# Optimization experiments

Hardware: AMD Instinct MI355X
Metric: run time of the kernel (lower is better)

The kernel has to match this reference:

```python
import jax, jax.numpy as jnp
import numpy as np

NUM_HEADS = 8
NEG_INF = -2**32 + 1  # matches the TF code's masking constant


def setup_inputs() -> dict:
    key = jax.random.key(0)
    ks = jax.random.split(key, 12)
    B, L, D_IN, D_MODEL = 2, 2048, 256, 256
    s = 1.0 / np.sqrt(D_IN)
    return {
        "queries": jax.random.normal(ks[0], (B, L, D_IN), jnp.float32),
        "keys": jax.random.normal(ks[1], (B, L, D_IN), jnp.float32),
        "values": jax.random.normal(ks[2], (B, L, D_IN), jnp.float32),
        "key_mask": jax.random.randint(ks[3], (B, L, 1), 0, 2, jnp.int32),
        "Wq": jax.random.normal(ks[4], (D_IN, D_MODEL), jnp.float32) * s,
        "bq": jnp.zeros((D_MODEL,), jnp.float32),
        "Wk": jax.random.normal(ks[5], (D_IN, D_MODEL), jnp.float32) * s,
        "bk": jnp.zeros((D_MODEL,), jnp.float32),
        "Wv": jax.random.normal(ks[6], (D_IN, D_MODEL), jnp.float32) * s,
        "bv": jnp.zeros((D_MODEL,), jnp.float32),
        "Wo": jax.random.normal(ks[7], (D_MODEL, D_IN), jnp.float32) * s,
        "bo": jnp.zeros((D_IN,), jnp.float32),
    }


def reference(queries, keys, values, key_mask, Wq, bq, Wk, bk, Wv, bv, Wo, bo):
    B, Lq, _ = queries.shape
    Lk = keys.shape[1]
    h = NUM_HEADS
    d_model = Wq.shape[1]
    depth = d_model // h

    Q = queries @ Wq + bq  # [B, Lq, d_model]
    K = keys @ Wk + bk     # [B, Lk, d_model]
    V = values @ Wv + bv   # [B, Lk, d_model]

    # split heads: contiguous chunks of size depth along feature dim
    Qh = Q.reshape(B, Lq, h, depth)
    Kh = K.reshape(B, Lk, h, depth)
    Vh = V.reshape(B, Lk, h, depth)

    scores = jnp.einsum("bqhd,bkhd->bhqk", Qh, Kh) / jnp.sqrt(
        jnp.asarray(depth, jnp.float32)
    )  # [B, h, Lq, Lk]

    # key_mask: [B, Lk, 1] -> broadcast over heads and query positions
    mask = (key_mask[:, None, :, 0] != 0)[:, :, None, :]  # [B, 1, 1, Lk]
    scores = jnp.where(mask, scores, jnp.asarray(NEG_INF, scores.dtype))

    attn = jax.nn.softmax(scores, axis=-1)  # dropout is identity at inference
    out = jnp.einsum("bhqk,bkhd->bqhd", attn, Vh).reshape(B, Lq, d_model)
    return out @ Wo + bo  # [B, Lq, input_dim]
```

## Files before the change

### kernel.cpp

```cpp
#include <hip/hip_runtime.h>

#define Bn 2
#define Ln 2048
#define DIN 256
#define Hn 8
#define DEPTH 32
#define SCALE 0.17677669529663687f
#define NEGC (-4294967296.0f)
#define NG  (Ln / 16)
#define WLS 264

typedef _Float16 f16;
typedef _Float16 h8 __attribute__((ext_vector_type(8)));
typedef _Float16 h4 __attribute__((ext_vector_type(4)));
typedef float f4 __attribute__((ext_vector_type(4)));


__global__ __launch_bounds__(256) void proj_gemm(
    const float* __restrict__ Xq, const float* __restrict__ Xk, const float* __restrict__ Xv,
    const float* __restrict__ Wq, const float* __restrict__ Wk, const float* __restrict__ Wv,
    const float* __restrict__ bq, const float* __restrict__ bk, const float* __restrict__ bv,
    f16* __restrict__ Qz, f16* __restrict__ Kz, f16* __restrict__ Vz)
{
    __shared__ f16 Wl[64 * WLS];
    const int p = blockIdx.z;
    const float* X = p == 0 ? Xq : p == 1 ? Xk : Xv;
    const float* W = p == 0 ? Wq : p == 1 ? Wk : Wv;
    const float* bias = p == 0 ? bq : p == 1 ? bk : bv;

    const int t = threadIdx.x, w = t >> 6, lane = t & 63;
    const int l15 = lane & 15, quad = lane >> 4;
    const int n0 = blockIdx.y * 64;

    {
        const int nl = t & 63, kb = t >> 6;
        for (int kk = 0; kk < 64; ++kk) {
            const int k = kk * 4 + kb;
            Wl[nl * WLS + k] = (f16)W[(size_t)k * DIN + n0 + nl];
        }
    }
    __syncthreads();

    const int m0w = blockIdx.x * 128 + w * 32;
    const float* A0 = X + (size_t)(m0w + l15) * DIN;
    const float* A1 = X + (size_t)(m0w + 16 + l15) * DIN;

    f4 acc[2][4];
    #pragma unroll
    for (int mi = 0; mi < 2; ++mi)
        #pragma unroll
        for (int tt = 0; tt < 4; ++tt) acc[mi][tt] = (f4){0.f, 0.f, 0.f, 0.f};

    for (int k0 = 0; k0 < DIN; k0 += 32) {
        float4 xa0 = *(const float4*)(A0 + k0 + quad * 8);
        float4 xb0 = *(const float4*)(A0 + k0 + quad * 8 + 4);
        float4 xa1 = *(const float4*)(A1 + k0 + quad * 8);
        float4 xb1 = *(const float4*)(A1 + k0 + quad * 8 + 4);
        h8 af0 = { (f16)xa0.x, (f16)xa0.y, (f16)xa0.z, (f16)xa0.w,
                   (f16)xb0.x, (f16)xb0.y, (f16)xb0.z, (f16)xb0.w };
        h8 af1 = { (f16)xa1.x, (f16)xa1.y, (f16)xa1.z, (f16)xa1.w,
                   (f16)xb1.x, (f16)xb1.y, (f16)xb1.z, (f16)xb1.w };
        #pragma unroll
        for (int tt = 0; tt < 4; ++tt) {
            h8 bf = *(const h8*)(Wl + (tt * 16 + l15) * WLS + k0 + quad * 8);
            acc[0][tt] = __builtin_amdgcn_mfma_f32_16x16x32_f16(af0, bf, acc[0][tt], 0, 0, 0);
            acc[1][tt] = __builtin_amdgcn_mfma_f32_16x16x32_f16(af1, bf, acc[1][tt], 0, 0, 0);
        }
    }
    #pragma unroll
    for (int mi = 0; mi < 2; ++mi)
        #pragma unroll
        for (int tt = 0; tt < 4; ++tt) {
            const int c = n0 + tt * 16 + l15;
            const float bb = bias[c];
            const int h = c >> 5, dd = c & 31;
            #pragma unroll
            for (int r = 0; r < 4; ++r) {
                const int row = m0w + mi * 16 + quad * 4 + r;
                const int b = row >> 11, l = row & (Ln - 1);
                const float v = acc[mi][tt][r] + bb;
                const size_t hbg = (size_t)(b * Hn + h) * NG + (l >> 4);
                if (p == 0)
                    Qz[(hbg * 64 + (dd >> 3) * 16 + (l & 15)) * 8 + (dd & 7)] =
                        (f16)(v * SCALE);
                else if (p == 1)
                    Kz[(hbg * 64 + (dd >> 3) * 16 + (l & 15)) * 8 + (dd & 7)] = (f16)v;
                else
                    Vz[((hbg * 2 + (dd >> 4)) * 64 + ((l & 15) >> 2) * 16 + (dd & 15)) * 4
                       + (l & 3)] = (f16)v;
            }
        }
}

__global__ __launch_bounds__(256) void flash_mfma(
    const f16* __restrict__ Qz, const f16* __restrict__ Kz,
    const f16* __restrict__ Vz, const int* __restrict__ mask,
    f16* __restrict__ Oz)
{
    __shared__ float Os[4][32][34];
    __shared__ float lS[4][32];
    const int t = threadIdx.x, w = t >> 6, lane = t & 63;
    const int l15 = lane & 15, quad = lane >> 4;
    const int qc = blockIdx.x, hb = blockIdx.y;
    const int q0 = qc * 32;
    const int b = hb >> 3, h = hb & 7;
    const f16* Qh = Qz + (size_t)hb * NG * 512;
    const f16* Kh = Kz + (size_t)hb * NG * 512;
    const f16* Vh = Vz + (size_t)hb * NG * 512;
    const int* mrow = mask + b * Ln;
    const int k_base = w * (Ln / 4);

    h8 qf[2];
    #pragma unroll
    for (int qg = 0; qg < 2; ++qg)
        qf[qg] = *(const h8*)(Qh + ((size_t)(qc * 2 + qg) * 64 + lane) * 8);

    f4 o[2][2];
    #pragma unroll
    for (int i = 0; i < 2; ++i)
        #pragma unroll
        for (int j = 0; j < 2; ++j) o[i][j] = (f4){0.f, 0.f, 0.f, 0.f};
    float l_run[2] = {0.f, 0.f};

    for (int kt = 0; kt < Ln / 4 / 64; ++kt) {
        const int k0 = k_base + kt * 64;
        #pragma unroll
        for (int tt = 0; tt < 4; ++tt) {
            const int g = (k0 >> 4) + tt;
            h8 kf = *(const h8*)(Kh + ((size_t)g * 64 + lane) * 8);
            const int4 mk = *(const int4*)(mrow + g * 16 + quad * 4);
            f4 bias4 = { mk.x ? 0.f : NEGC, mk.y ? 0.f : NEGC,
                         mk.z ? 0.f : NEGC, mk.w ? 0.f : NEGC };
            h4 va0 = *(const h4*)(Vh + ((size_t)(g * 2)     * 64 + lane) * 4);
            h4 va1 = *(const h4*)(Vh + ((size_t)(g * 2 + 1) * 64 + lane) * 4);
            f4 s[2];
            #pragma unroll
            for (int qg = 0; qg < 2; ++qg)
                s[qg] = __builtin_amdgcn_mfma_f32_16x16x32_f16(kf, qf[qg], bias4, 0, 0, 0);
            #pragma unroll
            for (int qg = 0; qg < 2; ++qg) {
                h4 pf;
                #pragma unroll
                for (int r = 0; r < 4; ++r) {
                    const float pv = __expf(s[qg][r]);
                    l_run[qg] += pv;
                    pf[r] = (f16)pv;
                }
                o[0][qg] = __builtin_amdgcn_mfma_f32_16x16x16f16(va0, pf, o[0][qg], 0, 0, 0);
                o[1][qg] = __builtin_amdgcn_mfma_f32_16x16x16f16(va1, pf, o[1][qg], 0, 0, 0);
            }
        }
    }
    #pragma unroll
    for (int qg = 0; qg < 2; ++qg) {
        l_run[qg] += __shfl_xor(l_run[qg], 16, 64);
        l_run[qg] += __shfl_xor(l_run[qg], 32, 64);
        if (quad == 0) lS[w][qg * 16 + l15] = l_run[qg];
        #pragma unroll
        for (int dg = 0; dg < 2; ++dg)
            #pragma unroll
            for (int r = 0; r < 4; ++r)
                Os[w][dg * 16 + quad * 4 + r][qg * 16 + l15] = o[dg][qg][r];
    }
    __syncthreads();

    if (t < 128) {
        const int cq = t & 31, dv = t >> 5;
        const float ls = lS[0][cq] + lS[1][cq] + lS[2][cq] + lS[3][cq];
        const float inv = 1.0f / ls;
        h8 pack;
        #pragma unroll
        for (int i = 0; i < 8; ++i) {
            const int dd = dv * 8 + i;
            const float ov = Os[0][dd][cq] + Os[1][dd][cq] +
                             Os[2][dd][cq] + Os[3][dd][cq];
            pack[i] = (f16)(ov * inv);
        }
        const int gm = b * NG + ((q0 + cq) >> 4);
        *(h8*)(Oz + (((size_t)gm * 8 + h) * 64 + dv * 16 + (cq & 15)) * 8) = pack;
    }
}

__global__ __launch_bounds__(256) void out_gemm(
    const f16* __restrict__ Oz, const float* __restrict__ Wo,
    const float* __restrict__ bo, float* __restrict__ out)
{
    const int t = threadIdx.x, w = t >> 6, lane = t & 63;
    const int l15 = lane & 15, quad = lane >> 4;
    const int g = blockIdx.x;

    h8 af[8];
    #pragma unroll
    for (int h = 0; h < 8; ++h)
        af[h] = *(const h8*)(Oz + (((size_t)g * 8 + h) * 64 + lane) * 8);

    const float* Wop = Wo + w * 64 + l15;
    f4 acc[4] = {{0.f,0.f,0.f,0.f},{0.f,0.f,0.f,0.f},
                 {0.f,0.f,0.f,0.f},{0.f,0.f,0.f,0.f}};
    #pragma unroll
    for (int h = 0; h < 8; ++h) {
        h8 bf[4];
        #pragma unroll
        for (int tt = 0; tt < 4; ++tt)
            #pragma unroll
            for (int j = 0; j < 8; ++j)
                bf[tt][j] = (f16)Wop[(size_t)(h * 32 + quad * 8 + j) * DIN + tt * 16];
        #pragma unroll
        for (int tt = 0; tt < 4; ++tt)
            acc[tt] = __builtin_amdgcn_mfma_f32_16x16x32_f16(af[h], bf[tt], acc[tt], 0, 0, 0);
    }
    #pragma unroll
    for (int tt = 0; tt < 4; ++tt) {
        const int c = w * 64 + tt * 16 + l15;
        const float bb = bo[c];
        #pragma unroll
        for (int r = 0; r < 4; ++r)
            out[(size_t)(g * 16 + quad * 4 + r) * DIN + c] = acc[tt][r] + bb;
    }
}

__global__ __launch_bounds__(256) void fb_projKV(
    const float* __restrict__ Xk, const float* __restrict__ Xv,
    const float* __restrict__ Wk, const float* __restrict__ Wv,
    const float* __restrict__ bk, const float* __restrict__ bv,
    f16* S, int b)
{
    __shared__ f16 Wl[64 * WLS];
    const int p = blockIdx.z;
    const float* X = (p ? Xv : Xk) + (size_t)b * Ln * DIN;
    const float* W = p ? Wv : Wk;
    const float* bias = p ? bv : bk;

    const int t = threadIdx.x, w = t >> 6, lane = t & 63;
    const int l15 = lane & 15, quad = lane >> 4;
    const int n0 = blockIdx.y * 64;

    {
        const int nl = t & 63, kb = t >> 6;
        for (int kk = 0; kk < 64; ++kk) {
            const int k = kk * 4 + kb;
            Wl[nl * WLS + k] = (f16)W[(size_t)k * DIN + n0 + nl];
        }
    }
    __syncthreads();

    const int m0w = blockIdx.x * 128 + w * 32;
    const float* A0 = X + (size_t)(m0w + l15) * DIN;
    const float* A1 = X + (size_t)(m0w + 16 + l15) * DIN;

    f4 acc[2][4];
    #pragma unroll
    for (int mi = 0; mi < 2; ++mi)
        #pragma unroll
        for (int tt = 0; tt < 4; ++tt) acc[mi][tt] = (f4){0.f, 0.f, 0.f, 0.f};

    for (int k0 = 0; k0 < DIN; k0 += 32) {
        float4 xa0 = *(const float4*)(A0 + k0 + quad * 8);
        float4 xb0 = *(const float4*)(A0 + k0 + quad * 8 + 4);
        float4 xa1 = *(const float4*)(A1 + k0 + quad * 8);
        float4 xb1 = *(const float4*)(A1 + k0 + quad * 8 + 4);
        h8 af0 = { (f16)xa0.x, (f16)xa0.y, (f16)xa0.z, (f16)xa0.w,
                   (f16)xb0.x, (f16)xb0.y, (f16)xb0.z, (f16)xb0.w };
        h8 af1 = { (f16)xa1.x, (f16)xa1.y, (f16)xa1.z, (f16)xa1.w,
                   (f16)xb1.x, (f16)xb1.y, (f16)xb1.z, (f16)xb1.w };
        #pragma unroll
        for (int tt = 0; tt < 4; ++tt) {
            h8 bf = *(const h8*)(Wl + (tt * 16 + l15) * WLS + k0 + quad * 8);
            acc[0][tt] = __builtin_amdgcn_mfma_f32_16x16x32_f16(af0, bf, acc[0][tt], 0, 0, 0);
            acc[1][tt] = __builtin_amdgcn_mfma_f32_16x16x32_f16(af1, bf, acc[1][tt], 0, 0, 0);
        }
    }
    #pragma unroll
    for (int mi = 0; mi < 2; ++mi)
        #pragma unroll
        for (int tt = 0; tt < 4; ++tt) {
            const int c = n0 + tt * 16 + l15;
            const float bb = bias[c];
            const int h = c >> 5, dd = c & 31;
            #pragma unroll
            for (int r = 0; r < 4; ++r) {
                const int l = m0w + mi * 16 + quad * 4 + r;
                const float v = acc[mi][tt][r] + bb;
                const unsigned hg = (unsigned)h * 128 + (l >> 4);
                unsigned j;
                if (!p)
                    j = (hg * 64 + (unsigned)(dd >> 3) * 16 + (l & 15)) * 8 + (dd & 7);
                else
                    j = 524288u + ((hg * 2 + (dd >> 4)) * 64
                        + (unsigned)((l & 15) >> 2) * 16 + (dd & 15)) * 4 + (l & 3);
                S[(((size_t)(j >> 12)) << 13) + 4096u + (j & 4095u)] = (f16)v;
            }
        }
}

__global__ __launch_bounds__(512) void fb_flashQ(
    const float* __restrict__ Xq, const float* __restrict__ Wq,
    const float* __restrict__ bq, const int* __restrict__ mask,
    float* outbuf, int b)
{
    __shared__ union {
        struct { f16 Wlq[32 * WLS]; f16 Qs[2048]; } a;
        struct { float Os[8][32][68]; float lS[8][64]; } c;
    } sm;
    f16* S = (f16*)outbuf;
    const int t = threadIdx.x, w = t >> 6, lane = t & 63;
    const int l15 = lane & 15, quad = lane >> 4;
    const int h = blockIdx.x, q0 = blockIdx.y * 64;

    {
        const int nl = t & 31, kb = t >> 5;
        for (int kk = 0; kk < 16; ++kk) {
            const int k = kk * 16 + kb;
            sm.a.Wlq[nl * WLS + k] = (f16)Wq[(size_t)k * DIN + h * 32 + nl];
        }
    }
    __syncthreads();

    if (w < 4) {
        const float* A0 = Xq + (size_t)(b * Ln + q0 + w * 16 + l15) * DIN;
        f4 a2[2] = { {0.f,0.f,0.f,0.f}, {0.f,0.f,0.f,0.f} };
        #pragma unroll
        for (int kk = 0; kk < 8; ++kk) {
            const int k0 = kk * 32;
            float4 xa = *(const float4*)(A0 + k0 + quad * 8);
            float4 xb = *(const float4*)(A0 + k0 + quad * 8 + 4);
            h8 af = { (f16)xa.x, (f16)xa.y, (f16)xa.z, (f16)xa.w,
                      (f16)xb.x, (f16)xb.y, (f16)xb.z, (f16)xb.w };
            #pragma unroll
            for (int tt = 0; tt < 2; ++tt) {
                h8 bf = *(const h8*)(sm.a.Wlq + (tt * 16 + l15) * WLS + k0 + quad * 8);
                a2[tt] = __builtin_amdgcn_mfma_f32_16x16x32_f16(af, bf, a2[tt], 0, 0, 0);
            }
        }
        #pragma unroll
        for (int tt = 0; tt < 2; ++tt) {
            const int c = tt * 16 + l15;
            const float bb = bq[h * 32 + c];
            #pragma unroll
            for (int r = 0; r < 4; ++r) {
                const int lc = quad * 4 + r;
                sm.a.Qs[((size_t)w * 64 + (c >> 3) * 16 + lc) * 8 + (c & 7)] =
                    (f16)((a2[tt][r] + bb) * SCALE);
            }
        }
    }
    __syncthreads();
    h8 qf[4];
    #pragma unroll
    for (int qg = 0; qg < 4; ++qg)
        qf[qg] = *(const h8*)(sm.a.Qs + ((size_t)qg * 64 + lane) * 8);
    __syncthreads();

    const int* mrow = mask + b * Ln;
    f4 o[2][4];
    #pragma unroll
    for (int i = 0; i < 2; ++i)
        #pragma unroll
        for (int j = 0; j < 4; ++j) o[i][j] = (f4){0.f, 0.f, 0.f, 0.f};
    float l_run[4] = {0.f, 0.f, 0.f, 0.f};
    const int k_base = w * (Ln / 8);

    for (int kt = 0; kt < Ln / 8 / 64; ++kt) {
        const int k0 = k_base + kt * 64;
        #pragma unroll
        for (int tt = 0; tt < 4; ++tt) {
            const int g = (k0 >> 4) + tt;
            const size_t kaddr = ((size_t)(h * 16 + (g >> 3)) << 13) + 4096u
                               + (size_t)((g & 7) * 512 + lane * 8);
            h8 kf = *(const h8*)(S + kaddr);
            const int4 mk = *(const int4*)(mrow + g * 16 + quad * 4);
            f4 bias4 = { mk.x ? 0.f : NEGC, mk.y ? 0.f : NEGC,
                         mk.z ? 0.f : NEGC, mk.w ? 0.f : NEGC };
            const size_t vaddr = ((size_t)(128 + h * 16 + (g >> 3)) << 13) + 4096u
                               + (size_t)((g & 7) * 512 + lane * 4);
            h4 va0 = *(const h4*)(S + vaddr);
            h4 va1 = *(const h4*)(S + vaddr + 256);
            f4 s_[4];
            #pragma unroll
            for (int qg = 0; qg < 4; ++qg)
                s_[qg] = __builtin_amdgcn_mfma_f32_16x16x32_f16(kf, qf[qg], bias4, 0, 0, 0);
            #pragma unroll
            for (int qg = 0; qg < 4; ++qg) {
                h4 pf;
                #pragma unroll
                for (int r = 0; r < 4; ++r) {
                    const float pv = __expf(s_[qg][r]);
                    l_run[qg] += pv;
                    pf[r] = (f16)pv;
                }
                o[0][qg] = __builtin_amdgcn_mfma_f32_16x16x16f16(va0, pf, o[0][qg], 0, 0, 0);
                o[1][qg] = __builtin_amdgcn_mfma_f32_16x16x16f16(va1, pf, o[1][qg], 0, 0, 0);
            }
        }
    }
    #pragma unroll
    for (int qg = 0; qg < 4; ++qg) {
        l_run[qg] += __shfl_xor(l_run[qg], 16, 64);
        l_run[qg] += __shfl_xor(l_run[qg], 32, 64);
        if (quad == 0) sm.c.lS[w][qg * 16 + l15] = l_run[qg];
        #pragma unroll
        for (int dg = 0; dg < 2; ++dg)
            #pragma unroll
            for (int r = 0; r < 4; ++r)
                sm.c.Os[w][dg * 16 + quad * 4 + r][qg * 16 + l15] = o[dg][qg][r];
    }
    __syncthreads();

    if (t < 256) {
        const int cq = t & 63, dv = t >> 6;
        float ls = 0.f;
        #pragma unroll
        for (int i = 0; i < 8; ++i) ls += sm.c.lS[i][cq];
        const float inv = 1.0f / ls;
        h8 pack;
        #pragma unroll
        for (int i = 0; i < 8; ++i) {
            const int dd = dv * 8 + i;
            float ov = 0.f;
            #pragma unroll
            for (int s = 0; s < 8; ++s) ov += sm.c.Os[s][dd][cq];
            pack[i] = (f16)(ov * inv);
        }
        const int gm = b * 128 + ((q0 + cq) >> 4);
        *(h8*)(S + (size_t)gm * 8192
               + (size_t)(h * 64 + dv * 16 + (cq & 15)) * 8) = pack;
    }
}

__global__ __launch_bounds__(256) void fb_outproj(
    const float* __restrict__ Wo, const float* __restrict__ bo, float* outbuf)
{
    f16* S = (f16*)outbuf;
    const int t = threadIdx.x, w = t >> 6, lane = t & 63;
    const int l15 = lane & 15, quad = lane >> 4;
    const int g = blockIdx.x;

    h8 af[8];
    #pragma unroll
    for (int h = 0; h < 8; ++h)
        af[h] = *(const h8*)(S + (size_t)g * 8192 + (size_t)(h * 64 + lane) * 8);
    __syncthreads();

    const float* Wop = Wo + w * 64 + l15;
    f4 acc[4] = {{0.f,0.f,0.f,0.f},{0.f,0.f,0.f,0.f},
                 {0.f,0.f,0.f,0.f},{0.f,0.f,0.f,0.f}};
    #pragma unroll
    for (int h = 0; h < 8; ++h) {
        h8 bf[4];
        #pragma unroll
        for (int tt = 0; tt < 4; ++tt)
            #pragma unroll
            for (int j = 0; j < 8; ++j)
                bf[tt][j] = (f16)Wop[(size_t)(h * 32 + quad * 8 + j) * DIN + tt * 16];
        #pragma unroll
        for (int tt = 0; tt < 4; ++tt)
            acc[tt] = __builtin_amdgcn_mfma_f32_16x16x32_f16(af[h], bf[tt], acc[tt], 0, 0, 0);
    }
    #pragma unroll
    for (int tt = 0; tt < 4; ++tt) {
        const int c = w * 64 + tt * 16 + l15;
        const float bb = bo[c];
        #pragma unroll
        for (int r = 0; r < 4; ++r)
            outbuf[(size_t)(g * 16 + quad * 4 + r) * DIN + c] = acc[tt][r] + bb;
    }
}

extern "C" void kernel_launch(void* const* d_in, const int* in_sizes, int n_in,
                              void* d_out, int out_size, void* d_ws, size_t ws_size,
                              hipStream_t stream) {
    (void)in_sizes; (void)n_in; (void)out_size;
    const float* Xq = (const float*)d_in[0];
    const float* Xk = (const float*)d_in[1];
    const float* Xv = (const float*)d_in[2];
    const int*  mask = (const int*)d_in[3];
    const float* Wq = (const float*)d_in[4];
    const float* bq = (const float*)d_in[5];
    const float* Wk = (const float*)d_in[6];
    const float* bk = (const float*)d_in[7];
    const float* Wv = (const float*)d_in[8];
    const float* bv = (const float*)d_in[9];
    const float* Wo = (const float*)d_in[10];
    const float* bo = (const float*)d_in[11];
    float* out = (float*)d_out;

    const size_t HB_E = (size_t)Bn * Hn * Ln * DEPTH;
    const size_t need = 4 * HB_E * sizeof(f16);

    if (ws_size >= need) {
        f16* Qz = (f16*)d_ws;
        f16* Kz = Qz + HB_E;
        f16* Vz = Kz + HB_E;
        f16* Oz = Vz + HB_E;
        proj_gemm<<<dim3(Bn * Ln / 128, DIN / 64, 3), 256, 0, stream>>>(
            Xq, Xk, Xv, Wq, Wk, Wv, bq, bk, bv, Qz, Kz, Vz);
        flash_mfma<<<dim3(Ln / 32, Bn * Hn), 256, 0, stream>>>(Qz, Kz, Vz, mask, Oz);
        out_gemm<<<Bn * Ln / 16, 256, 0, stream>>>(Oz, Wo, bo, out);
    } else {
        f16* S = (f16*)out;
        fb_projKV<<<dim3(16, 4, 2), 256, 0, stream>>>(Xk, Xv, Wk, Wv, bk, bv, S, 0);
        fb_flashQ<<<dim3(8, 32), 512, 0, stream>>>(Xq, Wq, bq, mask, out, 0);
        fb_projKV<<<dim3(16, 4, 2), 256, 0, stream>>>(Xk, Xv, Wk, Wv, bk, bv, S, 1);
        fb_flashQ<<<dim3(8, 32), 512, 0, stream>>>(Xq, Wq, bq, mask, out, 1);
        fb_outproj<<<256, 256, 0, stream>>>(Wo, bo, out);
    }
}
```

Before: 122.4 us.

## Split work finer across all three kernels and swizzle flash block order

The projection GEMM drops its shared-memory staging of W and reads W straight from global/cache per wave, halving rows per block so twice as many blocks launch. The flash kernel moves to 8 waves per block, each covering an eighth of the keys, with a 1D grid swizzled so consecutive blocks land on different XCDs. The output GEMM splits each row group's columns across two blocks. The aim is more parallelism and occupancy on a small problem, at the cost of more redundant W loads and a larger cross-wave reduction in shared memory.

```diff
diff --git a/kernel.cpp b/kernel.cpp
--- a/kernel.cpp
+++ b/kernel.cpp
@@ -22,7 +22,6 @@
     const float* __restrict__ bq, const float* __restrict__ bk, const float* __restrict__ bv,
     f16* __restrict__ Qz, f16* __restrict__ Kz, f16* __restrict__ Vz)
 {
-    __shared__ f16 Wl[64 * WLS];
     const int p = blockIdx.z;
     const float* X = p == 0 ? Xq : p == 1 ? Xk : Xv;
     const float* W = p == 0 ? Wq : p == 1 ? Wk : Wv;
@@ -31,84 +30,72 @@
     const int t = threadIdx.x, w = t >> 6, lane = t & 63;
     const int l15 = lane & 15, quad = lane >> 4;
     const int n0 = blockIdx.y * 64;
-
-    {
-        const int nl = t & 63, kb = t >> 6;
-        for (int kk = 0; kk < 64; ++kk) {
-            const int k = kk * 4 + kb;
-            Wl[nl * WLS + k] = (f16)W[(size_t)k * DIN + n0 + nl];
-        }
-    }
-    __syncthreads();
-
-    const int m0w = blockIdx.x * 128 + w * 32;
-    const float* A0 = X + (size_t)(m0w + l15) * DIN;
-    const float* A1 = X + (size_t)(m0w + 16 + l15) * DIN;
-
-    f4 acc[2][4];
-    #pragma unroll
-    for (int mi = 0; mi < 2; ++mi)
-        #pragma unroll
-        for (int tt = 0; tt < 4; ++tt) acc[mi][tt] = (f4){0.f, 0.f, 0.f, 0.f};
-
-    for (int k0 = 0; k0 < DIN; k0 += 32) {
-        float4 xa0 = *(const float4*)(A0 + k0 + quad * 8);
-        float4 xb0 = *(const float4*)(A0 + k0 + quad * 8 + 4);
-        float4 xa1 = *(const float4*)(A1 + k0 + quad * 8);
-        float4 xb1 = *(const float4*)(A1 + k0 + quad * 8 + 4);
-        h8 af0 = { (f16)xa0.x, (f16)xa0.y, (f16)xa0.z, (f16)xa0.w,
-                   (f16)xb0.x, (f16)xb0.y, (f16)xb0.z, (f16)xb0.w };
-        h8 af1 = { (f16)xa1.x, (f16)xa1.y, (f16)xa1.z, (f16)xa1.w,
-                   (f16)xb1.x, (f16)xb1.y, (f16)xb1.z, (f16)xb1.w };
-        #pragma unroll
-        for (int tt = 0; tt < 4; ++tt) {
-            h8 bf = *(const h8*)(Wl + (tt * 16 + l15) * WLS + k0 + quad * 8);
-            acc[0][tt] = __builtin_amdgcn_mfma_f32_16x16x32_f16(af0, bf, acc[0][tt], 0, 0, 0);
-            acc[1][tt] = __builtin_amdgcn_mfma_f32_16x16x32_f16(af1, bf, acc[1][tt], 0, 0, 0);
-        }
-    }
-    #pragma unroll
-    for (int mi = 0; mi < 2; ++mi)
-        #pragma unroll
-        for (int tt = 0; tt < 4; ++tt) {
-            const int c = n0 + tt * 16 + l15;
-            const float bb = bias[c];
-            const int h = c >> 5, dd = c & 31;
-            #pragma unroll
-            for (int r = 0; r < 4; ++r) {
-                const int row = m0w + mi * 16 + quad * 4 + r;
-                const int b = row >> 11, l = row & (Ln - 1);
-                const float v = acc[mi][tt][r] + bb;
-                const size_t hbg = (size_t)(b * Hn + h) * NG + (l >> 4);
-                if (p == 0)
-                    Qz[(hbg * 64 + (dd >> 3) * 16 + (l & 15)) * 8 + (dd & 7)] =
-                        (f16)(v * SCALE);
-                else if (p == 1)
-                    Kz[(hbg * 64 + (dd >> 3) * 16 + (l & 15)) * 8 + (dd & 7)] = (f16)v;
-                else
-                    Vz[((hbg * 2 + (dd >> 4)) * 64 + ((l & 15) >> 2) * 16 + (dd & 15)) * 4
-                       + (l & 3)] = (f16)v;
-            }
-        }
-}
-
-__global__ __launch_bounds__(256) void flash_mfma(
+    const int m0 = blockIdx.x * 64 + w * 16;
+
+    const float* A0 = X + (size_t)(m0 + l15) * DIN;
+    const float* Wp = W + n0 + l15;
+
+    f4 acc[4] = {{0.f,0.f,0.f,0.f},{0.f,0.f,0.f,0.f},
+                 {0.f,0.f,0.f,0.f},{0.f,0.f,0.f,0.f}};
+    #pragma unroll
+    for (int kk = 0; kk < 8; ++kk) {
+        const int k0 = kk * 32;
+        float4 xa = *(const float4*)(A0 + k0 + quad * 8);
+        float4 xb = *(const float4*)(A0 + k0 + quad * 8 + 4);
+        h8 af = { (f16)xa.x, (f16)xa.y, (f16)xa.z, (f16)xa.w,
+                  (f16)xb.x, (f16)xb.y, (f16)xb.z, (f16)xb.w };
+        h8 bf[4];
+        #pragma unroll
+        for (int tt = 0; tt < 4; ++tt)
+            #pragma unroll
+            for (int j = 0; j < 8; ++j)
+                bf[tt][j] = (f16)Wp[(size_t)(k0 + quad * 8 + j) * DIN + tt * 16];
+        #pragma unroll
+        for (int tt = 0; tt < 4; ++tt)
+            acc[tt] = __builtin_amdgcn_mfma_f32_16x16x32_f16(af, bf[tt], acc[tt], 0, 0, 0);
+    }
+    #pragma unroll
+    for (int tt = 0; tt < 4; ++tt) {
+        const int c = n0 + tt * 16 + l15;
+        const float bb = bias[c];
+        const int h = c >> 5, dd = c & 31;
+        #pragma unroll
+        for (int r = 0; r < 4; ++r) {
+            const int row = m0 + quad * 4 + r;
+            const int b = row >> 11, l = row & (Ln - 1);
+            const float v = acc[tt][r] + bb;
+            const size_t hbg = (size_t)(b * Hn + h) * NG + (l >> 4);
+            if (p == 0)
+                Qz[(hbg * 64 + (dd >> 3) * 16 + (l & 15)) * 8 + (dd & 7)] =
+                    (f16)(v * SCALE);
+            else if (p == 1)
+                Kz[(hbg * 64 + (dd >> 3) * 16 + (l & 15)) * 8 + (dd & 7)] = (f16)v;
+            else
+                Vz[((hbg * 2 + (dd >> 4)) * 64 + ((l & 15) >> 2) * 16 + (dd & 15)) * 4
+                   + (l & 3)] = (f16)v;
+        }
+    }
+}
+
+__global__ __launch_bounds__(512) void flash_mfma(
     const f16* __restrict__ Qz, const f16* __restrict__ Kz,
     const f16* __restrict__ Vz, const int* __restrict__ mask,
     f16* __restrict__ Oz)
 {
-    __shared__ float Os[4][32][34];
-    __shared__ float lS[4][32];
-    const int t = threadIdx.x, w = t >> 6, lane = t & 63;
-    const int l15 = lane & 15, quad = lane >> 4;
-    const int qc = blockIdx.x, hb = blockIdx.y;
+    __shared__ float Os[8][32][34];
+    __shared__ float lS[8][32];
+    const int t = threadIdx.x, w = t >> 6, lane = t & 63;
+    const int l15 = lane & 15, quad = lane >> 4;
+    const int bid = blockIdx.x;
+    const int swz = (bid & 7) * 128 + (bid >> 3);
+    const int hb = swz >> 6, qc = swz & 63;
     const int q0 = qc * 32;
     const int b = hb >> 3, h = hb & 7;
     const f16* Qh = Qz + (size_t)hb * NG * 512;
     const f16* Kh = Kz + (size_t)hb * NG * 512;
     const f16* Vh = Vz + (size_t)hb * NG * 512;
     const int* mrow = mask + b * Ln;
-    const int k_base = w * (Ln / 4);
+    const int k_base = w * (Ln / 8);
 
     h8 qf[2];
     #pragma unroll
@@ -122,7 +109,7 @@
         for (int j = 0; j < 2; ++j) o[i][j] = (f4){0.f, 0.f, 0.f, 0.f};
     float l_run[2] = {0.f, 0.f};
 
-    for (int kt = 0; kt < Ln / 4 / 64; ++kt) {
+    for (int kt = 0; kt < Ln / 8 / 64; ++kt) {
         const int k0 = k_base + kt * 64;
         #pragma unroll
         for (int tt = 0; tt < 4; ++tt) {
@@ -166,14 +153,17 @@
 
     if (t < 128) {
         const int cq = t & 31, dv = t >> 5;
-        const float ls = lS[0][cq] + lS[1][cq] + lS[2][cq] + lS[3][cq];
+        float ls = 0.f;
+        #pragma unroll
+        for (int i = 0; i < 8; ++i) ls += lS[i][cq];
         const float inv = 1.0f / ls;
         h8 pack;
         #pragma unroll
         for (int i = 0; i < 8; ++i) {
             const int dd = dv * 8 + i;
-            const float ov = Os[0][dd][cq] + Os[1][dd][cq] +
-                             Os[2][dd][cq] + Os[3][dd][cq];
+            float ov = 0.f;
+            #pragma unroll
+            for (int s = 0; s < 8; ++s) ov += Os[s][dd][cq];
             pack[i] = (f16)(ov * inv);
         }
         const int gm = b * NG + ((q0 + cq) >> 4);
@@ -187,31 +177,30 @@
 {
     const int t = threadIdx.x, w = t >> 6, lane = t & 63;
     const int l15 = lane & 15, quad = lane >> 4;
-    const int g = blockIdx.x;
+    const int g = blockIdx.x >> 1, nh = blockIdx.x & 1;
 
     h8 af[8];
     #pragma unroll
     for (int h = 0; h < 8; ++h)
         af[h] = *(const h8*)(Oz + (((size_t)g * 8 + h) * 64 + lane) * 8);
 
-    const float* Wop = Wo + w * 64 + l15;
-    f4 acc[4] = {{0.f,0.f,0.f,0.f},{0.f,0.f,0.f,0.f},
-                 {0.f,0.f,0.f,0.f},{0.f,0.f,0.f,0.f}};
+    const float* Wop = Wo + nh * 128 + w * 32 + l15;
+    f4 acc[2] = {{0.f,0.f,0.f,0.f},{0.f,0.f,0.f,0.f}};
     #pragma unroll
     for (int h = 0; h < 8; ++h) {
-        h8 bf[4];
-        #pragma unroll
-        for (int tt = 0; tt < 4; ++tt)
+        h8 bf[2];
+        #pragma unroll
+        for (int tt = 0; tt < 2; ++tt)
             #pragma unroll
             for (int j = 0; j < 8; ++j)
                 bf[tt][j] = (f16)Wop[(size_t)(h * 32 + quad * 8 + j) * DIN + tt * 16];
         #pragma unroll
-        for (int tt = 0; tt < 4; ++tt)
+        for (int tt = 0; tt < 2; ++tt)
             acc[tt] = __builtin_amdgcn_mfma_f32_16x16x32_f16(af[h], bf[tt], acc[tt], 0, 0, 0);
     }
     #pragma unroll
-    for (int tt = 0; tt < 4; ++tt) {
-        const int c = w * 64 + tt * 16 + l15;
+    for (int tt = 0; tt < 2; ++tt) {
+        const int c = nh * 128 + w * 32 + tt * 16 + l15;
         const float bb = bo[c];
         #pragma unroll
         for (int r = 0; r < 4; ++r)
@@ -492,10 +481,10 @@
         f16* Kz = Qz + HB_E;
         f16* Vz = Kz + HB_E;
         f16* Oz = Vz + HB_E;
-        proj_gemm<<<dim3(Bn * Ln / 128, DIN / 64, 3), 256, 0, stream>>>(
+        proj_gemm<<<dim3(Bn * Ln / 64, DIN / 64, 3), 256, 0, stream>>>(
             Xq, Xk, Xv, Wq, Wk, Wv, bq, bk, bv, Qz, Kz, Vz);
-        flash_mfma<<<dim3(Ln / 32, Bn * Hn), 256, 0, stream>>>(Qz, Kz, Vz, mask, Oz);
-        out_gemm<<<Bn * Ln / 16, 256, 0, stream>>>(Oz, Wo, bo, out);
+        flash_mfma<<<Ln / 32 * Bn * Hn, 512, 0, stream>>>(Qz, Kz, Vz, mask, Oz);
+        out_gemm<<<Bn * Ln / 16 * 2, 256, 0, stream>>>(Oz, Wo, bo, out);
     } else {
         f16* S = (f16*)out;
         fb_projKV<<<dim3(16, 4, 2), 256, 0, stream>>>(Xk, Xv, Wk, Wv, bk, bv, S, 0);
```

New measurement: 121.2 us. No clear change (-1.0%).
